# Optimization experiments

Hardware: AMD Instinct MI355X
Metric: run time of the kernel (lower is better)

Reference implementation:

```python
import jax, jax.numpy as jnp
import numpy as np

B, T, C, NH = 4, 2048, 1024, 16
HD = C // NH  # head dim = 64


def setup_inputs() -> dict:
    key = jax.random.key(0)
    k1, k2, k3 = jax.random.split(key, 3)
    x = jax.random.normal(k1, (B, T, C), dtype=jnp.float32)
    w_attn = jax.random.normal(k2, (C, 3 * C), dtype=jnp.float32) * (1.0 / np.sqrt(C))
    b_attn = jnp.zeros((3 * C,), dtype=jnp.float32)
    w_proj = jax.random.normal(k3, (C, C), dtype=jnp.float32) * (1.0 / np.sqrt(C))
    b_proj = jnp.zeros((C,), dtype=jnp.float32)
    return {"x": x, "w_attn": w_attn, "b_attn": b_attn, "w_proj": w_proj, "b_proj": b_proj}


def reference(x, w_attn, b_attn, w_proj, b_proj):
    Bx, Tx, Cx = x.shape
    # fused QKV projection
    qkv = x @ w_attn + b_attn              # [B, T, 3C]
    q, k, v = jnp.split(qkv, 3, axis=-1)   # each [B, T, C]
    # split heads: [B, NH, T, HD]
    q = q.reshape(Bx, Tx, NH, HD).transpose(0, 2, 1, 3)
    k = k.reshape(Bx, Tx, NH, HD).transpose(0, 2, 1, 3)
    v = v.reshape(Bx, Tx, NH, HD).transpose(0, 2, 1, 3)
    scale = 1.0 / np.sqrt(HD)
    att = jnp.einsum('bhqd,bhkd->bhqk', q, k) * scale  # [B, NH, T, T]
    causal = jnp.tril(jnp.ones((Tx, Tx), dtype=bool))
    att = jnp.where(causal[None, None], att, -jnp.inf)
    att = jax.nn.softmax(att, axis=-1)
    y = jnp.einsum('bhqk,bhkd->bhqd', att, v)           # [B, NH, T, HD]
    y = y.transpose(0, 2, 1, 3).reshape(Bx, Tx, Cx)
    return y @ w_proj + b_proj
```

## Files before the change

kernel.cpp:

```cpp
#include <hip/hip_runtime.h>
#include <hip/hip_bf16.h>

#define B_SZ 4
#define T_SZ 2048
#define C_SZ 1024
#define NH_SZ 16
#define HD_SZ 64
#define M_SZ (B_SZ * T_SZ)

typedef __bf16 bf16x8 __attribute__((ext_vector_type(8)));
typedef __bf16 bf16x4 __attribute__((ext_vector_type(4)));
typedef float f32x4 __attribute__((ext_vector_type(4)));

__device__ __forceinline__ void store_out(float* p, float v) { *p = v; }
__device__ __forceinline__ void store_out(__hip_bfloat16* p, float v) { *p = __float2bfloat16(v); }

__device__ __forceinline__ void async_ld16(__hip_bfloat16* lds, const __hip_bfloat16* g) {
  __builtin_amdgcn_global_load_lds(
      (const __attribute__((address_space(1))) void*)g,
      (__attribute__((address_space(3))) void*)lds, 16, 0, 0);
}

__device__ __forceinline__ void bar() {
  asm volatile("" ::: "memory");
  __builtin_amdgcn_s_barrier();
  asm volatile("" ::: "memory");
}

__global__ __launch_bounds__(256) void conv_bf16_kernel(
    const float* __restrict__ X, __hip_bfloat16* __restrict__ Y) {
  const int i = (blockIdx.x * 256 + threadIdx.x) * 4;
  float4 v = *(const float4*)&X[i];
  union { bf16x4 v; __hip_bfloat16 h[4]; } o;
  o.h[0] = __float2bfloat16(v.x); o.h[1] = __float2bfloat16(v.y);
  o.h[2] = __float2bfloat16(v.z); o.h[3] = __float2bfloat16(v.w);
  *(bf16x4*)&Y[i] = o.v;
}

template <int KD, int ND>
__global__ __launch_bounds__(256) void transpose_conv_kernel(
    const float* __restrict__ W, __hip_bfloat16* __restrict__ Wt) {
  __shared__ float sT[32][33];
  const int n0 = blockIdx.x * 32, k0 = blockIdx.y * 32;
  const int tid = threadIdx.x;
  {
    const int r = tid >> 3, c = (tid & 7) * 4;
    float4 v = *(const float4*)&W[(size_t)(k0 + r) * ND + n0 + c];
    sT[r][c] = v.x; sT[r][c + 1] = v.y; sT[r][c + 2] = v.z; sT[r][c + 3] = v.w;
  }
  __syncthreads();
  {
    const int n = tid >> 3, kq = (tid & 7) * 4;
    union { bf16x4 v; __hip_bfloat16 h[4]; } o;
#pragma unroll
    for (int j = 0; j < 4; ++j) o.h[j] = __float2bfloat16(sT[kq + j][n]);
    *(bf16x4*)&Wt[(size_t)(n0 + n) * KD + k0 + kq] = o.v;
  }
}

__device__ __forceinline__ bf16x8 lds_frag(const __hip_bfloat16* base, int row,
                                           int kk, int quad) {
  const int byte = row * 128 + (((kk << 6) | (quad << 4)) ^ ((row & 7) << 4));
  return *(const bf16x8*)((const char*)base + byte);
}

template <int N, int K, bool SPLIT, typename OutT>
__global__ __launch_bounds__(256, 2) void gemm_pipe_kernel(
    const __hip_bfloat16* __restrict__ A, const __hip_bfloat16* __restrict__ Bt,
    const float* __restrict__ bias, OutT* __restrict__ C,
    __hip_bfloat16* __restrict__ qR, __hip_bfloat16* __restrict__ kR,
    __hip_bfloat16* __restrict__ vT) {
  __shared__ __align__(16) __hip_bfloat16 sA[2][128 * 64];
  __shared__ __align__(16) __hip_bfloat16 sB[2][128 * 64];

  const int tid = threadIdx.x;
  const int wave = tid >> 6, lane = tid & 63;
  const int quad = lane >> 4, l16 = lane & 15;
  const int rw = (wave & 1) * 64, cw = (wave >> 1) * 64;

  constexpr int NBN = N / 128;
  constexpr int NBLK = (M_SZ / 128) * NBN;
  const int id = ((int)blockIdx.x & 7) * (NBLK / 8) + ((int)blockIdx.x >> 3);
  const int bm = (id / NBN) * 128, bn = (id % NBN) * 128;

  const int srow = tid >> 3;
  const int scol = ((((tid & 7) << 4) ^ ((srow & 7) << 4)) >> 1);
  const int sdst = tid * 8;
  const __hip_bfloat16* gA = A + (size_t)(bm + srow) * K + scol;
  const __hip_bfloat16* gB = Bt + (size_t)(bn + srow) * K + scol;

  f32x4 acc[4][4];
#pragma unroll
  for (int i = 0; i < 4; ++i)
#pragma unroll
    for (int j = 0; j < 4; ++j) acc[i][j] = (f32x4){0.f, 0.f, 0.f, 0.f};

#define STG128(buf, kt)                                                        \
  do {                                                                         \
    _Pragma("unroll") for (int ii = 0; ii < 4; ++ii) {                         \
      async_ld16(&sA[buf][ii * 2048 + sdst], gA + (size_t)(ii * 32) * K + (kt) * 64); \
      async_ld16(&sB[buf][ii * 2048 + sdst], gB + (size_t)(ii * 32) * K + (kt) * 64); \
    }                                                                          \
  } while (0)

  STG128(0, 0);
  asm volatile("s_waitcnt vmcnt(0)" ::: "memory");
  bar();

  constexpr int NT = K / 64;
  for (int kt = 0; kt < NT; ++kt) {
    if (kt + 1 < NT) STG128((kt + 1) & 1, kt + 1);
    const __hip_bfloat16* a_base = sA[kt & 1];
    const __hip_bfloat16* b_base = sB[kt & 1];

    bf16x8 af[4][2], bfr[4][2];
#pragma unroll
    for (int mq = 0; mq < 4; ++mq)
#pragma unroll
      for (int kk = 0; kk < 2; ++kk)
        af[mq][kk] = lds_frag(a_base, rw + mq * 16 + l16, kk, quad);
#pragma unroll
    for (int nq = 0; nq < 4; ++nq)
#pragma unroll
      for (int kk = 0; kk < 2; ++kk)
        bfr[nq][kk] = lds_frag(b_base, cw + nq * 16 + l16, kk, quad);
#pragma unroll
    for (int kk = 0; kk < 2; ++kk)
#pragma unroll
      for (int mq = 0; mq < 4; ++mq)
#pragma unroll
        for (int nq = 0; nq < 4; ++nq)
          acc[mq][nq] = __builtin_amdgcn_mfma_f32_16x16x32_bf16(
              af[mq][kk], bfr[nq][kk], acc[mq][nq], 0, 0, 0);

    asm volatile("s_waitcnt vmcnt(0)" ::: "memory");
    bar();
  }
#undef STG128

#pragma unroll
  for (int i = 0; i < 4; ++i)
#pragma unroll
    for (int j = 0; j < 4; ++j) {
      const int col = bn + cw + j * 16 + l16;
      const float bv = bias[col];
#pragma unroll
      for (int r = 0; r < 4; ++r) {
        const int row = bm + rw + i * 16 + quad * 4 + r;
        const float val = acc[i][j][r] + bv;
        if (SPLIT) {
          const int bb = row >> 11, t = row & 2047;
          const int hh = (col >> 6) & 15, d = col & 63;
          const int bh64 = bb * 16 + hh;
          if (col < C_SZ) {
            qR[((size_t)bh64 * T_SZ + t) * HD_SZ + d] = __float2bfloat16(val * 0.125f);
          } else if (col < 2 * C_SZ) {
            kR[((size_t)bh64 * T_SZ + t) * HD_SZ + d] = __float2bfloat16(val);
          } else {
            vT[((size_t)bh64 * HD_SZ + d) * T_SZ + t] = __float2bfloat16(val);
          }
        } else {
          store_out(&C[(size_t)row * N + col], val);
        }
      }
    }
}

#define ATT_ST 72

__global__ __launch_bounds__(256, 4) void attn_mfma_kernel(
    const __hip_bfloat16* __restrict__ qR, const __hip_bfloat16* __restrict__ kR,
    const __hip_bfloat16* __restrict__ vT, __hip_bfloat16* __restrict__ y) {
  __shared__ __align__(16) __hip_bfloat16 sQ[64][ATT_ST];
  __shared__ __align__(16) __hip_bfloat16 sK[64][ATT_ST];
  __shared__ __align__(16) __hip_bfloat16 sVt[64][ATT_ST];
  __shared__ __align__(16) __hip_bfloat16 sP[64][ATT_ST];

  const int bh = blockIdx.x;
  const int tile = (int)gridDim.y - 1 - blockIdx.y;
  const int t0 = tile * 64;
  const int tid = threadIdx.x;
  const int wave = tid >> 6, lane = tid & 63;
  const int quad = lane >> 4, l16 = lane & 15;
  const int wrow0 = wave * 16;

  const __hip_bfloat16* qb = qR + (size_t)bh * T_SZ * HD_SZ;
  const __hip_bfloat16* kb = kR + (size_t)bh * T_SZ * HD_SZ;
  const __hip_bfloat16* vb = vT + (size_t)bh * HD_SZ * T_SZ;

  const int sr = tid >> 2, sc = (tid & 3) * 16;

  {
    const __hip_bfloat16* src = qb + (size_t)t0 * HD_SZ + tid * 16;
    *(float4*)&sQ[sr][sc] = *(const float4*)src;
    *(float4*)&sQ[sr][sc + 8] = *(const float4*)(src + 8);
  }

  float4 krg0, krg1, vrg0, vrg1;
  {
    const __hip_bfloat16* ks = kb + tid * 16;
    krg0 = *(const float4*)ks;
    krg1 = *(const float4*)(ks + 8);
    const __hip_bfloat16* vs = vb + (size_t)sr * T_SZ + sc;
    vrg0 = *(const float4*)vs;
    vrg1 = *(const float4*)(vs + 8);
  }

  __syncthreads();
  bf16x8 qa0 = *(const bf16x8*)&sQ[wrow0 + l16][quad * 8];
  bf16x8 qa1 = *(const bf16x8*)&sQ[wrow0 + l16][32 + quad * 8];

  float lp[4];
  f32x4 o[4];
#pragma unroll
  for (int r = 0; r < 4; ++r) lp[r] = 0.f;
#pragma unroll
  for (int nn = 0; nn < 4; ++nn) o[nn] = (f32x4){0.f, 0.f, 0.f, 0.f};

  for (int j0 = 0; j0 <= t0; j0 += 64) {
    *(float4*)&sK[sr][sc] = krg0;
    *(float4*)&sK[sr][sc + 8] = krg1;
    *(float4*)&sVt[sr][sc] = vrg0;
    *(float4*)&sVt[sr][sc + 8] = vrg1;
    if (j0 + 64 <= t0) {
      const __hip_bfloat16* ks = kb + (size_t)(j0 + 64) * HD_SZ + tid * 16;
      krg0 = *(const float4*)ks;
      krg1 = *(const float4*)(ks + 8);
      const __hip_bfloat16* vs = vb + (size_t)sr * T_SZ + j0 + 64 + sc;
      vrg0 = *(const float4*)vs;
      vrg1 = *(const float4*)(vs + 8);
    }
    __syncthreads();

    f32x4 s[4];
#pragma unroll
    for (int sub = 0; sub < 4; ++sub) {
      s[sub] = (f32x4){0.f, 0.f, 0.f, 0.f};
      bf16x8 kf0 = *(const bf16x8*)&sK[sub * 16 + l16][quad * 8];
      s[sub] = __builtin_amdgcn_mfma_f32_16x16x32_bf16(qa0, kf0, s[sub], 0, 0, 0);
      bf16x8 kf1 = *(const bf16x8*)&sK[sub * 16 + l16][32 + quad * 8];
      s[sub] = __builtin_amdgcn_mfma_f32_16x16x32_bf16(qa1, kf1, s[sub], 0, 0, 0);
    }

    if (j0 == t0) {
#pragma unroll
      for (int sub = 0; sub < 4; ++sub) {
        const int key_l = sub * 16 + l16;
#pragma unroll
        for (int r = 0; r < 4; ++r) {
          const int row_l = wrow0 + quad * 4 + r;
          if (key_l > row_l) s[sub][r] = -1e30f;
        }
      }
    }

#pragma unroll
    for (int sub = 0; sub < 4; ++sub)
#pragma unroll
      for (int r = 0; r < 4; ++r) s[sub][r] = __expf(s[sub][r]);
#pragma unroll
    for (int r = 0; r < 4; ++r)
      lp[r] += (s[0][r] + s[1][r]) + (s[2][r] + s[3][r]);

#pragma unroll
    for (int sub = 0; sub < 4; ++sub)
#pragma unroll
      for (int r = 0; r < 4; ++r)
        sP[wrow0 + quad * 4 + r][sub * 16 + l16] = __float2bfloat16(s[sub][r]);

    bf16x8 pa0 = *(const bf16x8*)&sP[wrow0 + l16][quad * 8];
    bf16x8 pa1 = *(const bf16x8*)&sP[wrow0 + l16][32 + quad * 8];

#pragma unroll
    for (int nn = 0; nn < 4; ++nn) {
      bf16x8 vf0 = *(const bf16x8*)&sVt[nn * 16 + l16][quad * 8];
      o[nn] = __builtin_amdgcn_mfma_f32_16x16x32_bf16(pa0, vf0, o[nn], 0, 0, 0);
      bf16x8 vf1 = *(const bf16x8*)&sVt[nn * 16 + l16][32 + quad * 8];
      o[nn] = __builtin_amdgcn_mfma_f32_16x16x32_bf16(pa1, vf1, o[nn], 0, 0, 0);
    }

    if (j0 < t0) __syncthreads();
  }

#pragma unroll
  for (int off = 1; off <= 8; off <<= 1)
#pragma unroll
    for (int r = 0; r < 4; ++r) lp[r] += __shfl_xor(lp[r], off);
  float inv[4];
#pragma unroll
  for (int r = 0; r < 4; ++r) inv[r] = 1.0f / lp[r];

  const int b = bh >> 4, h = bh & 15;
#pragma unroll
  for (int nn = 0; nn < 4; ++nn)
#pragma unroll
    for (int r = 0; r < 4; ++r) {
      const int t = t0 + wrow0 + quad * 4 + r;
      y[((size_t)b * T_SZ + t) * C_SZ + h * HD_SZ + nn * 16 + l16] =
          __float2bfloat16(o[nn][r] * inv[r]);
    }
}

extern "C" void kernel_launch(void* const* d_in, const int* in_sizes, int n_in,
                              void* d_out, int out_size, void* d_ws, size_t ws_size,
                              hipStream_t stream) {
  const float* x      = (const float*)d_in[0];
  const float* w_attn = (const float*)d_in[1];
  const float* b_attn = (const float*)d_in[2];
  const float* w_proj = (const float*)d_in[3];
  const float* b_proj = (const float*)d_in[4];
  float* out = (float*)d_out;

  __hip_bfloat16* xb  = (__hip_bfloat16*)d_ws;
  __hip_bfloat16* waT = xb + (size_t)M_SZ * C_SZ;
  __hip_bfloat16* wpT = waT + (size_t)3 * C_SZ * C_SZ;
  __hip_bfloat16* qR  = wpT + (size_t)C_SZ * C_SZ;
  __hip_bfloat16* kR  = qR + (size_t)M_SZ * C_SZ;
  __hip_bfloat16* vT  = kR + (size_t)M_SZ * C_SZ;
  __hip_bfloat16* yb  = xb;

  conv_bf16_kernel<<<(M_SZ * C_SZ) / (256 * 4), 256, 0, stream>>>(x, xb);
  transpose_conv_kernel<C_SZ, 3 * C_SZ><<<dim3(96, 32), 256, 0, stream>>>(w_attn, waT);
  transpose_conv_kernel<C_SZ, C_SZ><<<dim3(32, 32), 256, 0, stream>>>(w_proj, wpT);

  gemm_pipe_kernel<3 * C_SZ, C_SZ, true, __hip_bfloat16>
      <<<dim3(1536), 256, 0, stream>>>(xb, waT, b_attn, nullptr, qR, kR, vT);

  attn_mfma_kernel<<<dim3(B_SZ * NH_SZ, T_SZ / 64), 256, 0, stream>>>(qR, kR, vT, yb);

  gemm_pipe_kernel<C_SZ, C_SZ, false, float>
      <<<dim3(512), 256, 0, stream>>>(yb, wpT, b_proj, out, nullptr, nullptr, nullptr);
}
```

Baseline: 282.6 us.

## Split QKV GEMM into 256-tile QK kernel and triple-buffered 128-tile kernels

Replaces the double-buffered 128x128, K=64 GEMM with triple-buffered kernels using K=32 stages and a two-stage-ahead prefetch with partial vmcnt waits. The Q/K part of the QKV projection now uses 256x256 tiles with 512 threads for more operand reuse. V and the output projection use a separate 128-tile kernel with a new XCD-aware block mapping. This aims to hide load latency and cut global traffic, at the cost of an extra launch, higher register pressure in the 256 tile, and more barriers per K step.

```diff
diff --git a/kernel.cpp b/kernel.cpp
--- a/kernel.cpp
+++ b/kernel.cpp
@@ -12,9 +12,6 @@
 typedef __bf16 bf16x4 __attribute__((ext_vector_type(4)));
 typedef float f32x4 __attribute__((ext_vector_type(4)));
 
-__device__ __forceinline__ void store_out(float* p, float v) { *p = v; }
-__device__ __forceinline__ void store_out(__hip_bfloat16* p, float v) { *p = __float2bfloat16(v); }
-
 __device__ __forceinline__ void async_ld16(__hip_bfloat16* lds, const __hip_bfloat16* g) {
   __builtin_amdgcn_global_load_lds(
       (const __attribute__((address_space(1))) void*)g,
@@ -25,6 +22,11 @@
   asm volatile("" ::: "memory");
   __builtin_amdgcn_s_barrier();
   asm volatile("" ::: "memory");
+}
+
+__device__ __forceinline__ bf16x8 frag32(const __hip_bfloat16* base, int row, int q) {
+  const int byte = (row << 6) + (((q ^ (row >> 1)) & 3) << 4);
+  return *(const bf16x8*)((const char*)base + byte);
 }
 
 __global__ __launch_bounds__(256) void conv_bf16_kernel(
@@ -58,36 +60,120 @@
   }
 }
 
-__device__ __forceinline__ bf16x8 lds_frag(const __hip_bfloat16* base, int row,
-                                           int kk, int quad) {
-  const int byte = row * 128 + (((kk << 6) | (quad << 4)) ^ ((row & 7) << 4));
-  return *(const bf16x8*)((const char*)base + byte);
-}
-
-template <int N, int K, bool SPLIT, typename OutT>
-__global__ __launch_bounds__(256, 2) void gemm_pipe_kernel(
+
+__global__ __launch_bounds__(512, 2) void gemm_tri256_qk(
     const __hip_bfloat16* __restrict__ A, const __hip_bfloat16* __restrict__ Bt,
-    const float* __restrict__ bias, OutT* __restrict__ C,
-    __hip_bfloat16* __restrict__ qR, __hip_bfloat16* __restrict__ kR,
+    const float* __restrict__ bias,
+    __hip_bfloat16* __restrict__ qR, __hip_bfloat16* __restrict__ kR) {
+  __shared__ __align__(16) __hip_bfloat16 sA[3][256 * 32];
+  __shared__ __align__(16) __hip_bfloat16 sB[3][256 * 32];
+
+  const int tid = threadIdx.x;
+  const int wave = tid >> 6, lane = tid & 63;
+  const int quad = lane >> 4, l16 = lane & 15;
+  const int wm = wave >> 2, wn = wave & 3;
+
+  const int xcd = (int)blockIdx.x & 7, lb = (int)blockIdx.x >> 3;
+  const int bm = (xcd * 4 + (lb >> 3)) * 256;
+  const int bn = (lb & 7) * 256;
+
+  const int srow = tid >> 2;
+  const int scol = 8 * ((tid & 3) ^ ((tid >> 3) & 3));
+  const int sdst = tid * 8;
+  const __hip_bfloat16* gA = A + (size_t)(bm + srow) * C_SZ + scol;
+  const __hip_bfloat16* gB = Bt + (size_t)(bn + srow) * C_SZ + scol;
+
+  f32x4 acc[8][4];
+#pragma unroll
+  for (int m = 0; m < 8; ++m)
+#pragma unroll
+    for (int n = 0; n < 4; ++n) acc[m][n] = (f32x4){0.f, 0.f, 0.f, 0.f};
+
+#define STG256(buf, kt)                                                         \
+  do {                                                                          \
+    async_ld16(&sA[buf][sdst], gA + (kt) * 32);                                 \
+    async_ld16(&sA[buf][4096 + sdst], gA + (size_t)128 * C_SZ + (kt) * 32);     \
+    async_ld16(&sB[buf][sdst], gB + (kt) * 32);                                 \
+    async_ld16(&sB[buf][4096 + sdst], gB + (size_t)128 * C_SZ + (kt) * 32);     \
+  } while (0)
+
+  STG256(0, 0);
+  STG256(1, 1);
+  asm volatile("s_waitcnt vmcnt(4)" ::: "memory");
+  bar();
+
+  constexpr int NT = C_SZ / 32;
+  int cur = 0;
+  for (int kt = 0; kt < NT; ++kt) {
+    const int stg = cur == 0 ? 2 : cur - 1;
+    if (kt + 2 < NT) STG256(stg, kt + 2);
+
+    const __hip_bfloat16* ab = sA[cur];
+    const __hip_bfloat16* bb = sB[cur];
+    bf16x8 af[8], bfr[4];
+#pragma unroll
+    for (int mq = 0; mq < 8; ++mq) af[mq] = frag32(ab, wm * 128 + mq * 16 + l16, quad);
+#pragma unroll
+    for (int nq = 0; nq < 4; ++nq) bfr[nq] = frag32(bb, wn * 64 + nq * 16 + l16, quad);
+#pragma unroll
+    for (int mq = 0; mq < 8; ++mq)
+#pragma unroll
+      for (int nq = 0; nq < 4; ++nq)
+        acc[mq][nq] = __builtin_amdgcn_mfma_f32_16x16x32_bf16(af[mq], bfr[nq], acc[mq][nq], 0, 0, 0);
+
+    if (kt + 1 < NT) {
+      if (kt + 2 < NT) asm volatile("s_waitcnt vmcnt(4)" ::: "memory");
+      else             asm volatile("s_waitcnt vmcnt(0)" ::: "memory");
+      bar();
+    }
+    cur = cur == 2 ? 0 : cur + 1;
+  }
+#undef STG256
+
+  float bv[4];
+#pragma unroll
+  for (int nq = 0; nq < 4; ++nq) bv[nq] = bias[bn + wn * 64 + nq * 16 + l16];
+  const bool isQ = bn < C_SZ;
+#pragma unroll
+  for (int mq = 0; mq < 8; ++mq)
+#pragma unroll
+    for (int nq = 0; nq < 4; ++nq) {
+      const int col = bn + wn * 64 + nq * 16 + l16;
+      const int hh = (col >> 6) & 15, d = col & 63;
+#pragma unroll
+      for (int r = 0; r < 4; ++r) {
+        const int row = bm + wm * 128 + mq * 16 + quad * 4 + r;
+        const int bb_ = row >> 11, t = row & 2047;
+        const size_t idx = ((size_t)(bb_ * 16 + hh) * T_SZ + t) * HD_SZ + d;
+        const float val = acc[mq][nq][r] + bv[nq];
+        if (isQ) qR[idx] = __float2bfloat16(val * 0.125f);
+        else     kR[idx] = __float2bfloat16(val);
+      }
+    }
+}
+
+template <int MODE>
+__global__ __launch_bounds__(256, 3) void gemm_tri128(
+    const __hip_bfloat16* __restrict__ A, const __hip_bfloat16* __restrict__ Bt,
+    const float* __restrict__ bias, float* __restrict__ Cf,
     __hip_bfloat16* __restrict__ vT) {
-  __shared__ __align__(16) __hip_bfloat16 sA[2][128 * 64];
-  __shared__ __align__(16) __hip_bfloat16 sB[2][128 * 64];
+  __shared__ __align__(16) __hip_bfloat16 sA[3][128 * 32];
+  __shared__ __align__(16) __hip_bfloat16 sB[3][128 * 32];
 
   const int tid = threadIdx.x;
   const int wave = tid >> 6, lane = tid & 63;
   const int quad = lane >> 4, l16 = lane & 15;
   const int rw = (wave & 1) * 64, cw = (wave >> 1) * 64;
 
-  constexpr int NBN = N / 128;
-  constexpr int NBLK = (M_SZ / 128) * NBN;
-  const int id = ((int)blockIdx.x & 7) * (NBLK / 8) + ((int)blockIdx.x >> 3);
-  const int bm = (id / NBN) * 128, bn = (id % NBN) * 128;
-
-  const int srow = tid >> 3;
-  const int scol = ((((tid & 7) << 4) ^ ((srow & 7) << 4)) >> 1);
+  const int xcd = (int)blockIdx.x & 7, lb = (int)blockIdx.x >> 3;
+  const int bm = (xcd * 8 + (lb >> 3)) * 128;
+  const int bn = (lb & 7) * 128;
+
+  const int srow = tid >> 2;
+  const int scol = 8 * ((tid & 3) ^ ((tid >> 3) & 3));
   const int sdst = tid * 8;
-  const __hip_bfloat16* gA = A + (size_t)(bm + srow) * K + scol;
-  const __hip_bfloat16* gB = Bt + (size_t)(bn + srow) * K + scol;
+  const __hip_bfloat16* gA = A + (size_t)(bm + srow) * C_SZ + scol;
+  const __hip_bfloat16* gB = Bt + (size_t)(bn + srow) * C_SZ + scol;
 
   f32x4 acc[4][4];
 #pragma unroll
@@ -97,70 +183,63 @@
 
 #define STG128(buf, kt)                                                        \
   do {                                                                         \
-    _Pragma("unroll") for (int ii = 0; ii < 4; ++ii) {                         \
-      async_ld16(&sA[buf][ii * 2048 + sdst], gA + (size_t)(ii * 32) * K + (kt) * 64); \
-      async_ld16(&sB[buf][ii * 2048 + sdst], gB + (size_t)(ii * 32) * K + (kt) * 64); \
-    }                                                                          \
+    async_ld16(&sA[buf][sdst], gA + (kt) * 32);                                \
+    async_ld16(&sA[buf][2048 + sdst], gA + (size_t)64 * C_SZ + (kt) * 32);     \
+    async_ld16(&sB[buf][sdst], gB + (kt) * 32);                                \
+    async_ld16(&sB[buf][2048 + sdst], gB + (size_t)64 * C_SZ + (kt) * 32);     \
   } while (0)
 
   STG128(0, 0);
-  asm volatile("s_waitcnt vmcnt(0)" ::: "memory");
+  STG128(1, 1);
+  asm volatile("s_waitcnt vmcnt(4)" ::: "memory");
   bar();
 
-  constexpr int NT = K / 64;
+  constexpr int NT = C_SZ / 32;
+  int cur = 0;
   for (int kt = 0; kt < NT; ++kt) {
-    if (kt + 1 < NT) STG128((kt + 1) & 1, kt + 1);
-    const __hip_bfloat16* a_base = sA[kt & 1];
-    const __hip_bfloat16* b_base = sB[kt & 1];
-
-    bf16x8 af[4][2], bfr[4][2];
+    const int stg = cur == 0 ? 2 : cur - 1;
+    if (kt + 2 < NT) STG128(stg, kt + 2);
+
+    const __hip_bfloat16* ab = sA[cur];
+    const __hip_bfloat16* bb = sB[cur];
+    bf16x8 af[4], bfr[4];
+#pragma unroll
+    for (int mq = 0; mq < 4; ++mq) af[mq] = frag32(ab, rw + mq * 16 + l16, quad);
+#pragma unroll
+    for (int nq = 0; nq < 4; ++nq) bfr[nq] = frag32(bb, cw + nq * 16 + l16, quad);
 #pragma unroll
     for (int mq = 0; mq < 4; ++mq)
 #pragma unroll
-      for (int kk = 0; kk < 2; ++kk)
-        af[mq][kk] = lds_frag(a_base, rw + mq * 16 + l16, kk, quad);
-#pragma unroll
-    for (int nq = 0; nq < 4; ++nq)
-#pragma unroll
-      for (int kk = 0; kk < 2; ++kk)
-        bfr[nq][kk] = lds_frag(b_base, cw + nq * 16 + l16, kk, quad);
-#pragma unroll
-    for (int kk = 0; kk < 2; ++kk)
-#pragma unroll
-      for (int mq = 0; mq < 4; ++mq)
-#pragma unroll
-        for (int nq = 0; nq < 4; ++nq)
-          acc[mq][nq] = __builtin_amdgcn_mfma_f32_16x16x32_bf16(
-              af[mq][kk], bfr[nq][kk], acc[mq][nq], 0, 0, 0);
-
-    asm volatile("s_waitcnt vmcnt(0)" ::: "memory");
-    bar();
+      for (int nq = 0; nq < 4; ++nq)
+        acc[mq][nq] = __builtin_amdgcn_mfma_f32_16x16x32_bf16(af[mq], bfr[nq], acc[mq][nq], 0, 0, 0);
+
+    if (kt + 1 < NT) {
+      if (kt + 2 < NT) asm volatile("s_waitcnt vmcnt(4)" ::: "memory");
+      else             asm volatile("s_waitcnt vmcnt(0)" ::: "memory");
+      bar();
+    }
+    cur = cur == 2 ? 0 : cur + 1;
   }
 #undef STG128
 
-#pragma unroll
-  for (int i = 0; i < 4; ++i)
-#pragma unroll
-    for (int j = 0; j < 4; ++j) {
-      const int col = bn + cw + j * 16 + l16;
-      const float bv = bias[col];
+  float bv[4];
+#pragma unroll
+  for (int nq = 0; nq < 4; ++nq) bv[nq] = bias[bn + cw + nq * 16 + l16];
+#pragma unroll
+  for (int mq = 0; mq < 4; ++mq)
+#pragma unroll
+    for (int nq = 0; nq < 4; ++nq) {
+      const int col = bn + cw + nq * 16 + l16;
 #pragma unroll
       for (int r = 0; r < 4; ++r) {
-        const int row = bm + rw + i * 16 + quad * 4 + r;
-        const float val = acc[i][j][r] + bv;
-        if (SPLIT) {
-          const int bb = row >> 11, t = row & 2047;
-          const int hh = (col >> 6) & 15, d = col & 63;
-          const int bh64 = bb * 16 + hh;
-          if (col < C_SZ) {
-            qR[((size_t)bh64 * T_SZ + t) * HD_SZ + d] = __float2bfloat16(val * 0.125f);
-          } else if (col < 2 * C_SZ) {
-            kR[((size_t)bh64 * T_SZ + t) * HD_SZ + d] = __float2bfloat16(val);
-          } else {
-            vT[((size_t)bh64 * HD_SZ + d) * T_SZ + t] = __float2bfloat16(val);
-          }
+        const int row = bm + rw + mq * 16 + quad * 4 + r;
+        const float val = acc[mq][nq][r] + bv[nq];
+        if (MODE == 0) {
+          const int bb_ = row >> 11, t = row & 2047;
+          const int hh = col >> 6, d = col & 63;
+          vT[((size_t)(bb_ * 16 + hh) * HD_SZ + d) * T_SZ + t] = __float2bfloat16(val);
         } else {
-          store_out(&C[(size_t)row * N + col], val);
+          Cf[(size_t)row * C_SZ + col] = val;
         }
       }
     }
@@ -323,11 +402,13 @@
   transpose_conv_kernel<C_SZ, 3 * C_SZ><<<dim3(96, 32), 256, 0, stream>>>(w_attn, waT);
   transpose_conv_kernel<C_SZ, C_SZ><<<dim3(32, 32), 256, 0, stream>>>(w_proj, wpT);
 
-  gemm_pipe_kernel<3 * C_SZ, C_SZ, true, __hip_bfloat16>
-      <<<dim3(1536), 256, 0, stream>>>(xb, waT, b_attn, nullptr, qR, kR, vT);
+  gemm_tri256_qk<<<dim3(256), 512, 0, stream>>>(xb, waT, b_attn, qR, kR);
+
+  gemm_tri128<0><<<dim3(512), 256, 0, stream>>>(
+      xb, waT + (size_t)2 * C_SZ * C_SZ, b_attn + 2 * C_SZ, nullptr, vT);
 
   attn_mfma_kernel<<<dim3(B_SZ * NH_SZ, T_SZ / 64), 256, 0, stream>>>(qR, kR, vT, yb);
 
-  gemm_pipe_kernel<C_SZ, C_SZ, false, float>
-      <<<dim3(512), 256, 0, stream>>>(yb, wpT, b_proj, out, nullptr, nullptr, nullptr);
-}
+  gemm_tri128<1><<<dim3(512), 256, 0, stream>>>(
+      (const __hip_bfloat16*)yb, wpT, b_proj, out, nullptr);
+}
```

New measurement: 265.2 us. -6.2%, faster.
